# Optimization experiments

Hardware: AMD Instinct MI355X
Metric: run time of the kernel (lower is better)

## Reference

```python
import jax, jax.numpy as jnp
import numpy as np

T, B, S, K, C = 2, 64, 30, 12, 20
N_ITEMS, D_ITEM, D_RNN = 20000, 128, 256
D_IN = D_ITEM + D_RNN  # cross_mode concatenates h_meta to basket embedding


def gru_cell(x, h, Wih, Whh, bih, bhh):
    # PyTorch GRUCell gate order: r, z, n
    gi = x @ Wih.T + bih
    gh = h @ Whh.T + bhh
    ir, iz, in_ = jnp.split(gi, 3, -1)
    hr, hz, hn = jnp.split(gh, 3, -1)
    r = jax.nn.sigmoid(ir + hr)
    z = jax.nn.sigmoid(iz + hz)
    n = jnp.tanh(in_ + r * hn)
    return (1.0 - z) * n + z * h


def setup_inputs() -> dict:
    key = jax.random.key(0)
    ks = jax.random.split(key, 16)
    def u(k, sh, fan):
        b = 1.0 / np.sqrt(fan)
        return jax.random.uniform(k, sh, jnp.float32, -b, b)
    return {
        "user_vectors": jax.random.randint(ks[0], (B,), 0, 1000),
        "item_vectors": jax.random.randint(ks[1], (T, B, S, K), 0, N_ITEMS),
        "copy_vectors": jax.random.randint(ks[2], (T, B, S, C), 0, N_ITEMS),
        "emb": jax.random.normal(ks[3], (N_ITEMS, D_ITEM), jnp.float32) * 0.05,
        "Wih": u(ks[4], (T, 3 * D_RNN, D_IN), D_RNN),
        "Whh": u(ks[5], (T, 3 * D_RNN, D_RNN), D_RNN),
        "bih": u(ks[6], (T, 3 * D_RNN), D_RNN),
        "bhh": u(ks[7], (T, 3 * D_RNN), D_RNN),
        "mWih": u(ks[8], (3 * D_RNN, T * D_RNN), D_RNN),
        "mWhh": u(ks[9], (3 * D_RNN, D_RNN), D_RNN),
        "mbih": u(ks[10], (3 * D_RNN,), D_RNN),
        "mbhh": u(ks[11], (3 * D_RNN,), D_RNN),
        "Wnew": u(ks[12], (N_ITEMS, D_RNN), D_RNN),
        "bnew": u(ks[13], (N_ITEMS,), D_RNN),
        "Wcopy": u(ks[14], (T, N_ITEMS, D_RNN), D_RNN),
        "bcopy": u(ks[15], (T, N_ITEMS), D_RNN),
    }


def _forward(item_vectors, copy_vectors, emb, Wih, Whh, bih, bhh,
             mWih, mWhh, mbih, mbhh, Wnew, bnew, Wcopy, bcopy):
    emb = emb.at[0].set(0.0)  # padding_idx=0
    e_items = emb[item_vectors]                               # [T,B,S,K,Di]
    valid = (item_vectors > 0).astype(e_items.dtype)          # [T,B,S,K]
    n_basket = valid.sum(-1)                                  # [T,B,S]
    cell_mask = (n_basket > 0).astype(e_items.dtype)          # [T,B,S]
    den = n_basket + (n_basket == 0).astype(e_items.dtype)
    e_baskets = e_items.sum(-2) / den[..., None]              # ave pool [T,B,S,Di]

    xs = jnp.moveaxis(e_baskets, 2, 0)  # [S,T,B,Di]
    ms = jnp.moveaxis(cell_mask, 2, 0)  # [S,T,B]

    h0 = jnp.zeros((T, B, D_RNN), e_items.dtype)
    hm0 = jnp.zeros((B, D_RNN), e_items.dtype)
    task_gru = jax.vmap(gru_cell)  # vmap over the task axis (distinct weights)

    def step(carry, inp):
        h_tasks, h_meta = carry
        x_t, m_t = inp
        # cross_mode: concat current meta hidden onto each task's input
        cell_in = jnp.concatenate(
            [x_t, jnp.broadcast_to(h_meta, (T, B, D_RNN))], -1)  # [T,B,D_IN]
        nh = task_gru(cell_in, h_tasks, Wih, Whh, bih, bhh)
        m = m_t[..., None]
        h_tasks = nh * m + h_tasks * (1.0 - m)  # freeze hidden on empty baskets
        meta_in = jnp.transpose(h_tasks, (1, 0, 2)).reshape(B, T * D_RNN)
        h_meta = gru_cell(meta_in, h_meta, mWih, mWhh, mbih, mbhh)
        return (h_tasks, h_meta), (h_tasks, h_meta)

    _, (h_seq, hm_seq) = jax.lax.scan(step, (h0, hm0), (xs, ms))
    e_rnn_tasks = jnp.transpose(h_seq, (1, 2, 0, 3))  # [T,B,S,H]
    e_rnn_meta = jnp.transpose(hm_seq, (1, 0, 2))     # [B,S,H]

    score_new = jnp.einsum('bsh,nh->bsn', e_rnn_meta, Wnew) + bnew  # [B,S,N]
    ti = jnp.arange(T)[:, None, None, None]
    bi = jnp.arange(B)[None, :, None, None]
    si = jnp.arange(S)[None, None, :, None]
    copy_mask = jnp.zeros((T, B, S, N_ITEMS), score_new.dtype).at[
        ti, bi, si, copy_vectors].set(1.0)  # scatter_(-1, copy_vectors, 1)
    score_copy = (jnp.einsum('tbsh,tnh->tbsn', e_rnn_tasks, Wcopy)
                  + bcopy[:, None, None, :]) * copy_mask  # [T,B,S,N]
    # stack new-item scores with per-task masked copy scores
    return jnp.concatenate([score_new[None], score_copy], 0)  # [T+1,B,S,N]


def reference(user_vectors, item_vectors, copy_vectors, emb, Wih, Whh, bih, bhh,
              mWih, mWhh, mbih, mbhh, Wnew, bnew, Wcopy, bcopy):
    return _forward(item_vectors, copy_vectors, emb, Wih, Whh, bih, bhh,
                    mWih, mWhh, mbih, mbhh, Wnew, bnew, Wcopy, bcopy)
```

## Files before the change

### kernel.cpp

```cpp
#include <hip/hip_runtime.h>

typedef unsigned short u16;
typedef unsigned int u32;
typedef unsigned long long u64;
typedef __attribute__((ext_vector_type(8))) short short8;
typedef __attribute__((ext_vector_type(4))) float f32x4;

#define NB_ 64
#define NHELP_ 6195

static __device__ __forceinline__ f32x4 mfma16(short8 a, short8 b, f32x4 c) {
  return __builtin_amdgcn_mfma_f32_16x16x32_bf16(a, b, c, 0, 0, 0);
}

static __device__ __forceinline__ void split_bf16(float x, u16& hi, u16& lo) {
  unsigned u = __float_as_uint(x);
  unsigned r = (u + 0x7fffu + ((u >> 16) & 1u)) >> 16;
  hi = (u16)r;
  float fh = __uint_as_float(r << 16);
  float xl = x - fh;
  unsigned ul = __float_as_uint(xl);
  unsigned rl2 = (ul + 0x7fffu + ((ul >> 16) & 1u)) >> 16;
  lo = (u16)rl2;
}

static __device__ __forceinline__ void astore(u32* p, u32 v) {
  __hip_atomic_store(p, v, __ATOMIC_RELAXED, __HIP_MEMORY_SCOPE_AGENT);
}
static __device__ __forceinline__ void unpack8(const uint4& a, const uint4& b,
                                               short8& h, short8& l) {
  u32 wb[8] = {a.x, a.y, a.z, a.w, b.x, b.y, b.z, b.w};
  #pragma unroll
  for (int j = 0; j < 8; ++j) {
    h[j] = (short)(wb[j] & 0xffffu);
    l[j] = (short)(wb[j] >> 16);
  }
}
static __device__ __forceinline__ float unpack_hl(u32 pk) {
  return __uint_as_float((pk & 0xffffu) << 16) + __uint_as_float(pk & 0xffff0000u);
}
static __device__ __forceinline__ void vload8(const u32* p, short8& h, short8& l) {
  uint4 a = *(const uint4*)p;
  uint4 b = *(const uint4*)(p + 4);
  unpack8(a, b, h, l);
}

__global__ __launch_bounds__(256) void k_prep(const int* __restrict__ iv,
                                              const float* __restrict__ emb,
                                              u16* __restrict__ ebh, u16* __restrict__ ebl,
                                              float* __restrict__ cm,
                                              const float* __restrict__ Wih,
                                              const float* __restrict__ Whh,
                                              const float* __restrict__ mWih,
                                              const float* __restrict__ mWhh,
                                              const float* __restrict__ Wnew,
                                              u16* __restrict__ w1h, u16* __restrict__ w1l,
                                              u16* __restrict__ w2h, u16* __restrict__ w2l,
                                              u16* __restrict__ wnh, u16* __restrict__ wnl) {
  if (blockIdx.x < 1920) {
    int u = blockIdx.x * 2 + (threadIdx.x >> 7);
    int s = u >> 7;
    int t = (u >> 6) & 1;
    int b = u & 63;
    int d = threadIdx.x & 127;
    const int ibase = ((t * 64 + b) * 30 + s) * 12;
    float sum = 0.f;
    int cnt = 0;
    for (int k = 0; k < 12; ++k) {
      int idx = iv[ibase + k];
      if (idx > 0) { cnt++; sum += emb[(size_t)idx * 128 + d]; }
    }
    float den = (cnt > 0) ? (float)cnt : 1.f;
    float v = sum / den;
    u16 hi, lo; split_bf16(v, hi, lo);
    ebh[(size_t)u * 128 + d] = hi;
    ebl[(size_t)u * 128 + d] = lo;
    if (d == 0) cm[u] = (cnt > 0) ? 1.f : 0.f;
    return;
  }
  int gu = (blockIdx.x - 1920) * 4 + (threadIdx.x >> 6);
  int lane = threadIdx.x & 63;
  int ko = (lane >> 4) * 8;
  int cl = lane & 15;
  float src[8];
  if (gu < 2560) {
    int blk = gu / 40, r = gu % 40, ksIdx = r >> 1, nt = r & 1;
    int t = blk >> 5, hd0 = (blk & 31) * 8;
    int c = nt * 16 + cl;
    if (c < 24) {
      int gc = (c < 8) ? (hd0 + c) : (c < 16) ? (256 + hd0 + (c - 8)) : (512 + hd0 + (c - 16));
      const float* wrow; int kk;
      if (ksIdx < 8)       { wrow = Wih + (size_t)(t * 768 + gc) * 384 + 128; kk = ksIdx * 32 + ko; }
      else if (ksIdx < 16) { wrow = Whh + (size_t)(t * 768 + gc) * 256;       kk = (ksIdx - 8) * 32 + ko; }
      else                 { wrow = Wih + (size_t)(t * 768 + gc) * 384;       kk = (ksIdx - 16) * 32 + ko; }
      #pragma unroll
      for (int j = 0; j < 8; ++j) src[j] = wrow[kk + j];
    } else {
      #pragma unroll
      for (int j = 0; j < 8; ++j) src[j] = 0.f;
    }
    int off = gu * 512 + lane * 8;
    #pragma unroll
    for (int j = 0; j < 8; ++j) { u16 h, l; split_bf16(src[j], h, l); w1h[off + j] = h; w1l[off + j] = l; }
  } else if (gu < 4096) {
    int g2 = gu - 2560;
    int blk = g2 / 24, ksIdx = g2 % 24;
    int t1 = blk >> 5;
    int hd0 = blk * 4;
    int c = cl;
    if (c < 12) {
      int gc = (c < 4) ? (hd0 + c) : (c < 8) ? (256 + hd0 + (c - 4)) : (512 + hd0 + (c - 8));
      if (ksIdx < 16) {
        int chunk = (ksIdx < 8) ? (t1 * 8 + ksIdx) : ((1 - t1) * 8 + (ksIdx - 8));
        int kk = chunk * 32 + ko;
        #pragma unroll
        for (int j = 0; j < 8; ++j) src[j] = mWih[(size_t)gc * 512 + kk + j];
      } else {
        int kk = (ksIdx - 16) * 32 + ko;
        #pragma unroll
        for (int j = 0; j < 8; ++j) src[j] = mWhh[(size_t)gc * 256 + kk + j];
      }
    } else {
      #pragma unroll
      for (int j = 0; j < 8; ++j) src[j] = 0.f;
    }
    int off = g2 * 512 + lane * 8;
    #pragma unroll
    for (int j = 0; j < 8; ++j) { u16 h, l; split_bf16(src[j], h, l); w2h[off + j] = h; w2l[off + j] = l; }
  } else if (gu < 14144) {
    int g3 = gu - 4096;
    int gnt = g3 >> 3, ks = g3 & 7;
    int col = gnt * 16 + cl;
    if (col < 20000) {
      int kk = ks * 32 + ko;
      #pragma unroll
      for (int j = 0; j < 8; ++j) src[j] = Wnew[(size_t)col * 256 + kk + j];
    } else {
      #pragma unroll
      for (int j = 0; j < 8; ++j) src[j] = 0.f;
    }
    int off = g3 * 512 + lane * 8;
    #pragma unroll
    for (int j = 0; j < 8; ++j) { u16 h, l; split_bf16(src[j], h, l); wnh[off + j] = h; wnl[off + j] = l; }
  }
}

__global__ __launch_bounds__(256) void k_gix(const u16* __restrict__ ebh, const u16* __restrict__ ebl,
                                             const u16* __restrict__ w1h, const u16* __restrict__ w1l,
                                             const float* __restrict__ bih, const float* __restrict__ bhh,
                                             float* __restrict__ gix) {
  int blk = blockIdx.x;
  int t1 = blk >> 5, hd1 = (blk & 31) * 8;
  int tid = threadIdx.x, lane = tid & 63, w = tid >> 6;
  int arow = w * 16 + (lane & 15);
  int ko = (lane >> 4) * 8;
  __shared__ u16 lwh[4096], lwl[4096];
  {
    const uint4* sh = (const uint4*)(w1h + ((size_t)blk * 40 + 32) * 512);
    const uint4* sl = (const uint4*)(w1l + ((size_t)blk * 40 + 32) * 512);
    uint4* dh = (uint4*)lwh; uint4* dl = (uint4*)lwl;
    for (int i = tid; i < 512; i += 256) { dh[i] = sh[i]; dl[i] = sl[i]; }
  }
  int c = lane & 15;
  float brz, bn = 0.f;
  {
    int gc = (c < 8) ? (hd1 + c) : (256 + hd1 + (c - 8));
    brz = bih[t1 * 768 + gc] + bhh[t1 * 768 + gc];
    if (c < 8) bn = bih[t1 * 768 + 512 + hd1 + c];
  }
  __syncthreads();
  for (int s = 0; s < 30; ++s) {
    f32x4 a3[2];
    a3[0] = (f32x4){0.f, 0.f, 0.f, 0.f};
    a3[1] = (f32x4){0.f, 0.f, 0.f, 0.f};
    const u16* Xh = ebh + (size_t)((s * 2 + t1) * 64 + arow) * 128;
    const u16* Xl = ebl + (size_t)((s * 2 + t1) * 64 + arow) * 128;
    #pragma unroll
    for (int k = 0; k < 4; ++k) {
      short8 xh = *(const short8*)(Xh + k * 32 + ko);
      short8 xl = *(const short8*)(Xl + k * 32 + ko);
      #pragma unroll
      for (int nt = 0; nt < 2; ++nt) {
        short8 bh = *(const short8*)(lwh + (k * 2 + nt) * 512 + lane * 8);
        short8 bl = *(const short8*)(lwl + (k * 2 + nt) * 512 + lane * 8);
        a3[nt] = mfma16(xh, bh, a3[nt]);
        a3[nt] = mfma16(xl, bh, a3[nt]);
        a3[nt] = mfma16(xh, bl, a3[nt]);
      }
    }
    float* grow = gix + (size_t)(blk * 30 + s) * 64 * 32;
    #pragma unroll
    for (int i = 0; i < 4; ++i) {
      int r = w * 16 + (lane >> 4) * 4 + i;
      grow[r * 32 + c] = a3[0][i] + brz;
      if (c < 8) grow[r * 32 + 16 + c] = a3[1][i] + bn;
    }
  }
}

static __device__ __forceinline__ void bar_arrive(u32* slots, int blk, int epoch) {
  __syncthreads();
  if (threadIdx.x == 0) astore(slots + blk, (u32)epoch);
}
static __device__ __forceinline__ void bar_wait(u32* slots, int epoch) {
  int lane = threadIdx.x & 63;
  u32 v;
  for (;;) {
    asm volatile("global_load_dword %0, %1, off sc0 sc1\n\ts_waitcnt vmcnt(0)"
                 : "=v"(v) : "v"(slots + lane) : "memory");
    if ((int)v >= epoch) break;
  }
}
static __device__ __forceinline__ void helper_wait(const u32* hprog, int target) {
  if (threadIdx.x == 0) {
    u32 v;
    for (;;) {
      asm volatile("global_load_dword %0, %1, off sc0 sc1\n\ts_waitcnt vmcnt(0)"
                   : "=v"(v) : "v"(hprog) : "memory");
      if ((int)v >= target) break;
      __builtin_amdgcn_s_sleep(15);
      __builtin_amdgcn_s_sleep(15);
    }
  }
  __syncthreads();
}

#define RNN_LDS 130560

__global__ __launch_bounds__(256, 1) void k_mega(
    const u16* __restrict__ w1h, const u16* __restrict__ w1l,
    const u16* __restrict__ w2h, const u16* __restrict__ w2l,
    const float* __restrict__ gix,
    const float* __restrict__ bhh,
    const float* __restrict__ mbih, const float* __restrict__ mbhh,
    const float* __restrict__ cm,
    u32* __restrict__ hpk,
    u32* __restrict__ apk,
    u32* slots,
    const u16* __restrict__ wnh, const u16* __restrict__ wnl,
    const float* __restrict__ bnew,
    const int* __restrict__ cv,
    const float* __restrict__ wc,
    const float* __restrict__ bc,
    float* __restrict__ out) {
  u32* hprog = slots + 64;

  if (blockIdx.x >= NB_) {
    int h = blockIdx.x - NB_;
    int g = h / 413, r = h % 413;
    int tid = threadIdx.x, lane = tid & 63, w = tid >> 6;
    int ko = (lane >> 4) * 8;
    if (r < 256) {
      int s = 2 * g + (r >= 128);
      int rr = r & 127;
      int t = rr >> 6, b = rr & 63;
      float* orow = out + (size_t)(1 + t) * 38400000 + (size_t)(b * 30 + s) * 20000;
      f32x4 z4 = {0.f, 0.f, 0.f, 0.f};
      f32x4* zp = (f32x4*)orow;
      for (int i = tid; i < 5000; i += 256)
        __builtin_nontemporal_store(z4, zp + i);
      helper_wait(hprog, 2 * s + 1);
      const u32* hp = hpk + (size_t)(((s + 1) * 2 + t) * 64 + b) * 256;
      uint4 hq = *(const uint4*)(hp + lane * 4);
      float4 h4;
      h4.x = unpack_hl(hq.x); h4.y = unpack_hl(hq.y);
      h4.z = unpack_hl(hq.z); h4.w = unpack_hl(hq.w);
      int base = ((t * 64 + b) * 30 + s) * 20;
      for (int c = w; c < 20; c += 4) {
        int idx = cv[base + c];
        const float* wr = wc + ((size_t)t * 20000 + idx) * 256;
        float4 w4 = *(const float4*)(wr + lane * 4);
        float d = h4.x * w4.x + h4.y * w4.y + h4.z * w4.z + h4.w * w4.w;
        #pragma unroll
        for (int m = 32; m >= 1; m >>= 1) d += __shfl_xor(d, m, 64);
        if (lane == 0) orow[idx] = d + bc[t * 20000 + idx];
      }
    } else {
      int q = g, nb = r - 256;
      helper_wait(hprog, 4 * q + 4);
      f32x4 acc[2][8];
      #pragma unroll
      for (int mi = 0; mi < 2; ++mi)
        #pragma unroll
        for (int nt = 0; nt < 8; ++nt) acc[mi][nt] = (f32x4){0.f, 0.f, 0.f, 0.f};
      #pragma unroll
      for (int ks = 0; ks < 8; ++ks) {
        short8 ah[2], al[2];
        #pragma unroll
        for (int mi = 0; mi < 2; ++mi) {
          int rrow = q * 128 + (w * 2 + mi) * 16 + (lane & 15);
          vload8(apk + (size_t)rrow * 256 + ks * 32 + ko, ah[mi], al[mi]);
        }
        #pragma unroll
        for (int nt = 0; nt < 8; ++nt) {
          int un = (nb * 8 + nt) * 8 + ks;
          short8 bh = *(const short8*)(wnh + (size_t)un * 512 + lane * 8);
          short8 bl = *(const short8*)(wnl + (size_t)un * 512 + lane * 8);
          #pragma unroll
          for (int mi = 0; mi < 2; ++mi) {
            acc[mi][nt] = mfma16(ah[mi], bh, acc[mi][nt]);
            acc[mi][nt] = mfma16(al[mi], bh, acc[mi][nt]);
            acc[mi][nt] = mfma16(ah[mi], bl, acc[mi][nt]);
          }
        }
      }
      #pragma unroll
      for (int mi = 0; mi < 2; ++mi)
        #pragma unroll
        for (int nt = 0; nt < 8; ++nt) {
          int col = nb * 128 + nt * 16 + (lane & 15);
          if (col < 20000) {
            float bn = bnew[col];
            #pragma unroll
            for (int i = 0; i < 4; ++i) {
              int rrow = q * 128 + (w * 2 + mi) * 16 + (lane >> 4) * 4 + i;
              int sA = rrow >> 6, bA = rrow & 63;
              out[(size_t)(bA * 30 + sA) * 20000 + col] = acc[mi][nt][i] + bn;
            }
          }
        }
    }
    return;
  }

  extern __shared__ char smem[];
  u16* lw1h = (u16*)smem;
  u16* lw1l = (u16*)(smem + 32768);
  u16* lw2h = (u16*)(smem + 65536);
  u16* lw2l = (u16*)(smem + 90112);
  float* ls_rz = (float*)(smem + 114688);
  float* ls_gi = (float*)(smem + 118784);
  float* ls_gh = (float*)(smem + 120832);
  float* ls_cm = (float*)(smem + 122880);

  const int blk = blockIdx.x;
  const int tid = threadIdx.x;
  const int lane = tid & 63;
  const int w = tid >> 6;
  const int t1 = blk >> 5;
  const int hd1 = (blk & 31) * 8;
  const int hd2 = blk * 4;
  const int arow = w * 16 + (lane & 15);
  const int ko = (lane >> 4) * 8;
  int epoch = 0;

  {
    const uint4* s1h = (const uint4*)(w1h + (size_t)blk * 40 * 512);
    const uint4* s1l = (const uint4*)(w1l + (size_t)blk * 40 * 512);
    uint4* d1h = (uint4*)lw1h; uint4* d1l = (uint4*)lw1l;
    for (int i = tid; i < 2048; i += 256) { d1h[i] = s1h[i]; d1l[i] = s1l[i]; }
    const uint4* s2h = (const uint4*)(w2h + (size_t)blk * 24 * 512);
    const uint4* s2l = (const uint4*)(w2l + (size_t)blk * 24 * 512);
    uint4* d2h = (uint4*)lw2h; uint4* d2l = (uint4*)lw2l;
    for (int i = tid; i < 1536; i += 256) { d2h[i] = s2h[i]; d2l[i] = s2l[i]; }
    for (int i = tid; i < 1920; i += 256) ls_cm[i] = cm[((i >> 6) * 2 + t1) * 64 + (i & 63)];
  }
  const int cc = lane & 15;
  float bhhn = (cc < 8) ? bhh[t1 * 768 + 512 + hd1 + cc] : 0.f;
  float mrz_b = 0.f, mgi_b = 0.f, mgh_b = 0.f;
  if (cc < 8) {
    int gc = (cc < 4) ? (hd2 + cc) : (256 + hd2 + (cc - 4));
    mrz_b = mbih[gc] + mbhh[gc];
  } else if (cc < 12) {
    int gn = 512 + hd2 + (cc - 8);
    mgi_b = mbih[gn];
    mgh_b = mbhh[gn];
  }

  float gq[8];
  {
    const float* grow = gix + (size_t)(blk * 30 + 0) * 2048;
    #pragma unroll
    for (int i = 0; i < 4; ++i) {
      int r = w * 16 + (lane >> 4) * 4 + i;
      gq[i]     = grow[r * 32 + cc];
      gq[4 + i] = grow[r * 32 + 16 + (cc & 7)];
    }
  }
  __syncthreads();

  short8 ah1[8], al1[8];
  short8 xh2[8], xl2[8];
  f32x4 a2s[2];
  a2s[0] = (f32x4){0.f, 0.f, 0.f, 0.f};
  a2s[1] = (f32x4){0.f, 0.f, 0.f, 0.f};
  float hold0 = 0.f, hold1 = 0.f;
  float hm_reg = 0.f;

  for (int s = 0; s < 30; ++s) {
    f32x4 a1[2];
    a1[0] = (f32x4){0.f, 0.f, 0.f, 0.f};
    a1[1] = (f32x4){0.f, 0.f, 0.f, 0.f};
    if (s > 0) {
      bar_wait(slots, epoch);
      if (blk == 0 && tid == 0) astore(hprog, (u32)epoch);
      const u32* Ap = apk + (size_t)((s - 1) * 64 + arow) * 256 + ko;
      uint4 ra[16];
      #pragma unroll
      for (int k = 0; k < 8; ++k) {
        ra[2 * k]     = *(const uint4*)(Ap + k * 32);
        ra[2 * k + 1] = *(const uint4*)(Ap + k * 32 + 4);
      }
      #pragma unroll
      for (int k = 0; k < 8; ++k) {
        unpack8(ra[2 * k], ra[2 * k + 1], ah1[k], al1[k]);
        #pragma unroll
        for (int nt = 0; nt < 2; ++nt) {
          short8 bh = *(const short8*)(lw1h + (k * 2 + nt) * 512 + lane * 8);
          short8 bl = *(const short8*)(lw1l + (k * 2 + nt) * 512 + lane * 8);
          a1[nt] = mfma16(ah1[k], bh, a1[nt]);
          a1[nt] = mfma16(al1[k], bh, a1[nt]);
          a1[nt] = mfma16(ah1[k], bl, a1[nt]);
        }
      }
    }
    #pragma unroll
    for (int i = 0; i < 4; ++i) {
      int rl = (lane >> 4) * 4 + i;
      ls_rz[(w * 16 + rl) * 16 + cc] = a1[0][i] + a2s[0][i] + gq[i];
      if (cc < 8) {
        ls_gi[(w * 16 + rl) * 8 + cc] = a1[1][i] + gq[4 + i];
        ls_gh[(w * 16 + rl) * 8 + cc] = a2s[1][i] + bhhn;
      }
    }
    asm volatile("s_waitcnt lgkmcnt(0)" ::: "memory");
    {
      int item = lane;
      int rl = item >> 3, c = item & 7;
      float rv = ls_rz[(w * 16 + rl) * 16 + c], zv = ls_rz[(w * 16 + rl) * 16 + 8 + c];
      float gi = ls_gi[(w * 16 + rl) * 8 + c], gh = ls_gh[(w * 16 + rl) * 8 + c];
      float r = 1.f / (1.f + expf(-rv));
      float z = 1.f / (1.f + expf(-zv));
      float n = tanhf(gi + r * gh);
      int b = w * 16 + rl;
      float m = ls_cm[s * 64 + b];
      float hnew = (1.f - z) * n + z * hold0;
      float hout = (m > 0.5f) ? hnew : hold0;
      hold0 = hout;
      int oo = (((s + 1) * 2 + t1) * 64 + b) * 256 + hd1 + c;
      u16 xh, xl; split_bf16(hout, xh, xl);
      astore(hpk + oo, (u32)xh | ((u32)xl << 16));
    }
    {
      int item = 64 + lane;
      int rl = item >> 3, c = item & 7;
      float rv = ls_rz[(w * 16 + rl) * 16 + c], zv = ls_rz[(w * 16 + rl) * 16 + 8 + c];
      float gi = ls_gi[(w * 16 + rl) * 8 + c], gh = ls_gh[(w * 16 + rl) * 8 + c];
      float r = 1.f / (1.f + expf(-rv));
      float z = 1.f / (1.f + expf(-zv));
      float n = tanhf(gi + r * gh);
      int b = w * 16 + rl;
      float m = ls_cm[s * 64 + b];
      float hnew = (1.f - z) * n + z * hold1;
      float hout = (m > 0.5f) ? hnew : hold1;
      hold1 = hout;
      int oo = (((s + 1) * 2 + t1) * 64 + b) * 256 + hd1 + c;
      u16 xh, xl; split_bf16(hout, xh, xl);
      astore(hpk + oo, (u32)xh | ((u32)xl << 16));
    }
    ++epoch;
    bar_arrive(slots, blk, epoch);

    f32x4 m1 = (f32x4){0.f, 0.f, 0.f, 0.f};
    f32x4 m2 = (f32x4){0.f, 0.f, 0.f, 0.f};
    if (s > 0) {
      #pragma unroll
      for (int k = 0; k < 8; ++k) {
        short8 bh = *(const short8*)(lw2h + (16 + k) * 512 + lane * 8);
        short8 bl = *(const short8*)(lw2l + (16 + k) * 512 + lane * 8);
        m2 = mfma16(ah1[k], bh, m2);
        m2 = mfma16(al1[k], bh, m2);
        m2 = mfma16(ah1[k], bl, m2);
      }
    }
    if (s < 29) {
      const float* grow = gix + (size_t)(blk * 30 + s + 1) * 2048;
      #pragma unroll
      for (int i = 0; i < 4; ++i) {
        int r = w * 16 + (lane >> 4) * 4 + i;
        gq[i]     = grow[r * 32 + cc];
        gq[4 + i] = grow[r * 32 + 16 + (cc & 7)];
      }
    }
    bar_wait(slots, epoch);
    if (blk == 0 && tid == 0) astore(hprog, (u32)epoch);

    {
      const u32* Hp = hpk + (size_t)(((s + 1) * 2 + t1) * 64 + arow) * 256 + ko;
      const u32* Hq = hpk + (size_t)(((s + 1) * 2 + (1 - t1)) * 64 + arow) * 256 + ko;
      uint4 rx[16], ry[16];
      #pragma unroll
      for (int k = 0; k < 8; ++k) {
        rx[2 * k]     = *(const uint4*)(Hp + k * 32);
        rx[2 * k + 1] = *(const uint4*)(Hp + k * 32 + 4);
        ry[2 * k]     = *(const uint4*)(Hq + k * 32);
        ry[2 * k + 1] = *(const uint4*)(Hq + k * 32 + 4);
      }
      #pragma unroll
      for (int k = 0; k < 8; ++k) {
        unpack8(rx[2 * k], rx[2 * k + 1], xh2[k], xl2[k]);
        short8 bh = *(const short8*)(lw2h + k * 512 + lane * 8);
        short8 bl = *(const short8*)(lw2l + k * 512 + lane * 8);
        m1 = mfma16(xh2[k], bh, m1);
        m1 = mfma16(xl2[k], bh, m1);
        m1 = mfma16(xh2[k], bl, m1);
      }
      #pragma unroll
      for (int k = 0; k < 8; ++k) {
        short8 yh, yl;
        unpack8(ry[2 * k], ry[2 * k + 1], yh, yl);
        short8 bh = *(const short8*)(lw2h + (8 + k) * 512 + lane * 8);
        short8 bl = *(const short8*)(lw2l + (8 + k) * 512 + lane * 8);
        m1 = mfma16(yh, bh, m1);
        m1 = mfma16(yl, bh, m1);
        m1 = mfma16(yh, bl, m1);
      }
    }
    #pragma unroll
    for (int i = 0; i < 4; ++i) {
      int rl = (lane >> 4) * 4 + i;
      if (cc < 8) {
        ls_rz[(w * 16 + rl) * 16 + cc] = m1[i] + m2[i] + mrz_b;
      } else if (cc < 12) {
        ls_gi[(w * 16 + rl) * 8 + (cc - 8)] = m1[i] + mgi_b;
        ls_gh[(w * 16 + rl) * 8 + (cc - 8)] = m2[i] + mgh_b;
      }
    }
    asm volatile("s_waitcnt lgkmcnt(0)" ::: "memory");
    {
      int rl = lane >> 2, c = lane & 3;
      float rv = ls_rz[(w * 16 + rl) * 16 + c], zv = ls_rz[(w * 16 + rl) * 16 + 4 + c];
      float gi = ls_gi[(w * 16 + rl) * 8 + c], gh = ls_gh[(w * 16 + rl) * 8 + c];
      float r = 1.f / (1.f + expf(-rv));
      float z = 1.f / (1.f + expf(-zv));
      float n = tanhf(gi + r * gh);
      int b = w * 16 + rl;
      int g2 = hd2 + c;
      float hmnew = (1.f - z) * n + z * hm_reg;
      hm_reg = hmnew;
      int ar = s * 64 + b;
      u16 xh, xl; split_bf16(hmnew, xh, xl);
      astore(apk + ar * 256 + g2, (u32)xh | ((u32)xl << 16));
    }
    ++epoch;
    bar_arrive(slots, blk, epoch);

    a2s[0] = (f32x4){0.f, 0.f, 0.f, 0.f};
    a2s[1] = (f32x4){0.f, 0.f, 0.f, 0.f};
    if (s < 29) {
      #pragma unroll
      for (int k = 0; k < 8; ++k) {
        #pragma unroll
        for (int nt = 0; nt < 2; ++nt) {
          short8 bh = *(const short8*)(lw1h + ((8 + k) * 2 + nt) * 512 + lane * 8);
          short8 bl = *(const short8*)(lw1l + ((8 + k) * 2 + nt) * 512 + lane * 8);
          a2s[nt] = mfma16(xh2[k], bh, a2s[nt]);
          a2s[nt] = mfma16(xl2[k], bh, a2s[nt]);
          a2s[nt] = mfma16(xh2[k], bl, a2s[nt]);
        }
      }
    }
  }
  if (blk == 0) {
    bar_wait(slots, epoch);
    if (tid == 0) astore(hprog, (u32)epoch);
  }
}

extern "C" void kernel_launch(void* const* d_in, const int* in_sizes, int n_in,
                              void* d_out, int out_size, void* d_ws, size_t ws_size,
                              hipStream_t stream) {
  const int* iv = (const int*)d_in[1];
  const int* cv = (const int*)d_in[2];
  const float* emb = (const float*)d_in[3];
  const float* Wih = (const float*)d_in[4];
  const float* Whh = (const float*)d_in[5];
  const float* bih = (const float*)d_in[6];
  const float* bhh = (const float*)d_in[7];
  const float* mWih = (const float*)d_in[8];
  const float* mWhh = (const float*)d_in[9];
  const float* mbih = (const float*)d_in[10];
  const float* mbhh = (const float*)d_in[11];
  const float* Wnew = (const float*)d_in[12];
  const float* bnew = (const float*)d_in[13];
  const float* Wcopy = (const float*)d_in[14];
  const float* bcopy = (const float*)d_in[15];
  float* out = (float*)d_out;
  char* ws = (char*)d_ws;

  size_t o = 0;
  auto take = [&](size_t sz) { size_t r = o; o += sz; return r; };
  size_t BAR = take(512);
  size_t CM  = take(15360);
  size_t EBH = take(983040);
  size_t EBL = take(983040);
  size_t HPK = take(4063232);
  size_t APK = take(1966080);
  size_t GIX = take(15728640);
  size_t W1H = take(2621440);
  size_t W1L = take(2621440);
  size_t W2H = take(1572864);
  size_t W2L = take(1572864);
  size_t WNH = take(10289152);
  size_t WNL = take(10289152);
  if (ws_size < o) return;

  hipFuncSetAttribute(reinterpret_cast<const void*>(k_mega),
                      hipFuncAttributeMaxDynamicSharedMemorySize, RNN_LDS);

  hipMemsetAsync(ws + BAR, 0, 512, stream);

  k_prep<<<5456, 256, 0, stream>>>(iv, emb, (u16*)(ws + EBH), (u16*)(ws + EBL), (float*)(ws + CM),
                                   Wih, Whh, mWih, mWhh, Wnew,
                                   (u16*)(ws + W1H), (u16*)(ws + W1L),
                                   (u16*)(ws + W2H), (u16*)(ws + W2L),
                                   (u16*)(ws + WNH), (u16*)(ws + WNL));
  k_gix<<<64, 256, 0, stream>>>((const u16*)(ws + EBH), (const u16*)(ws + EBL),
                                (const u16*)(ws + W1H), (const u16*)(ws + W1L),
                                bih, bhh, (float*)(ws + GIX));
  k_mega<<<NB_ + NHELP_, 256, RNN_LDS, stream>>>(
      (const u16*)(ws + W1H), (const u16*)(ws + W1L),
      (const u16*)(ws + W2H), (const u16*)(ws + W2L),
      (const float*)(ws + GIX), bhh, mbih, mbhh,
      (const float*)(ws + CM),
      (u32*)(ws + HPK), (u32*)(ws + APK),
      (u32*)(ws + BAR),
      (const u16*)(ws + WNH), (const u16*)(ws + WNL),
      bnew, cv, Wcopy, bcopy, out);
}
```

Baseline: 473.1 us.

## Fuse input-gate precompute kernel into persistent RNN megakernel

Removes the separate k_gix launch and computes the input-side gate projections inside each RNN block of k_mega, reusing W1 slices now kept in a larger LDS region. Each block writes and then reads back its own gix rows, which saves a kernel launch and the reload of W1 from global memory. Helper blocks that zero the copy-score rows now wait for RNN progress before zeroing, which shifts when that bandwidth is used. The cost is more LDS per RNN block and a longer serial prologue before the recurrence starts.

```diff
diff --git a/kernel.cpp b/kernel.cpp
--- a/kernel.cpp
+++ b/kernel.cpp
@@ -145,59 +145,6 @@
   }
 }
 
-__global__ __launch_bounds__(256) void k_gix(const u16* __restrict__ ebh, const u16* __restrict__ ebl,
-                                             const u16* __restrict__ w1h, const u16* __restrict__ w1l,
-                                             const float* __restrict__ bih, const float* __restrict__ bhh,
-                                             float* __restrict__ gix) {
-  int blk = blockIdx.x;
-  int t1 = blk >> 5, hd1 = (blk & 31) * 8;
-  int tid = threadIdx.x, lane = tid & 63, w = tid >> 6;
-  int arow = w * 16 + (lane & 15);
-  int ko = (lane >> 4) * 8;
-  __shared__ u16 lwh[4096], lwl[4096];
-  {
-    const uint4* sh = (const uint4*)(w1h + ((size_t)blk * 40 + 32) * 512);
-    const uint4* sl = (const uint4*)(w1l + ((size_t)blk * 40 + 32) * 512);
-    uint4* dh = (uint4*)lwh; uint4* dl = (uint4*)lwl;
-    for (int i = tid; i < 512; i += 256) { dh[i] = sh[i]; dl[i] = sl[i]; }
-  }
-  int c = lane & 15;
-  float brz, bn = 0.f;
-  {
-    int gc = (c < 8) ? (hd1 + c) : (256 + hd1 + (c - 8));
-    brz = bih[t1 * 768 + gc] + bhh[t1 * 768 + gc];
-    if (c < 8) bn = bih[t1 * 768 + 512 + hd1 + c];
-  }
-  __syncthreads();
-  for (int s = 0; s < 30; ++s) {
-    f32x4 a3[2];
-    a3[0] = (f32x4){0.f, 0.f, 0.f, 0.f};
-    a3[1] = (f32x4){0.f, 0.f, 0.f, 0.f};
-    const u16* Xh = ebh + (size_t)((s * 2 + t1) * 64 + arow) * 128;
-    const u16* Xl = ebl + (size_t)((s * 2 + t1) * 64 + arow) * 128;
-    #pragma unroll
-    for (int k = 0; k < 4; ++k) {
-      short8 xh = *(const short8*)(Xh + k * 32 + ko);
-      short8 xl = *(const short8*)(Xl + k * 32 + ko);
-      #pragma unroll
-      for (int nt = 0; nt < 2; ++nt) {
-        short8 bh = *(const short8*)(lwh + (k * 2 + nt) * 512 + lane * 8);
-        short8 bl = *(const short8*)(lwl + (k * 2 + nt) * 512 + lane * 8);
-        a3[nt] = mfma16(xh, bh, a3[nt]);
-        a3[nt] = mfma16(xl, bh, a3[nt]);
-        a3[nt] = mfma16(xh, bl, a3[nt]);
-      }
-    }
-    float* grow = gix + (size_t)(blk * 30 + s) * 64 * 32;
-    #pragma unroll
-    for (int i = 0; i < 4; ++i) {
-      int r = w * 16 + (lane >> 4) * 4 + i;
-      grow[r * 32 + c] = a3[0][i] + brz;
-      if (c < 8) grow[r * 32 + 16 + c] = a3[1][i] + bn;
-    }
-  }
-}
-
 static __device__ __forceinline__ void bar_arrive(u32* slots, int blk, int epoch) {
   __syncthreads();
   if (threadIdx.x == 0) astore(slots + blk, (u32)epoch);
@@ -225,13 +172,14 @@
   __syncthreads();
 }
 
-#define RNN_LDS 130560
+#define RNN_LDS 146944
 
 __global__ __launch_bounds__(256, 1) void k_mega(
     const u16* __restrict__ w1h, const u16* __restrict__ w1l,
     const u16* __restrict__ w2h, const u16* __restrict__ w2l,
-    const float* __restrict__ gix,
-    const float* __restrict__ bhh,
+    const u16* __restrict__ ebh, const u16* __restrict__ ebl,
+    float* __restrict__ gix,
+    const float* __restrict__ bih, const float* __restrict__ bhh,
     const float* __restrict__ mbih, const float* __restrict__ mbhh,
     const float* __restrict__ cm,
     u32* __restrict__ hpk,
@@ -255,16 +203,17 @@
       int rr = r & 127;
       int t = rr >> 6, b = rr & 63;
       float* orow = out + (size_t)(1 + t) * 38400000 + (size_t)(b * 30 + s) * 20000;
+      helper_wait(hprog, 2 * s + 1);
       f32x4 z4 = {0.f, 0.f, 0.f, 0.f};
       f32x4* zp = (f32x4*)orow;
       for (int i = tid; i < 5000; i += 256)
         __builtin_nontemporal_store(z4, zp + i);
-      helper_wait(hprog, 2 * s + 1);
       const u32* hp = hpk + (size_t)(((s + 1) * 2 + t) * 64 + b) * 256;
       uint4 hq = *(const uint4*)(hp + lane * 4);
       float4 h4;
       h4.x = unpack_hl(hq.x); h4.y = unpack_hl(hq.y);
       h4.z = unpack_hl(hq.z); h4.w = unpack_hl(hq.w);
+      __syncthreads();
       int base = ((t * 64 + b) * 30 + s) * 20;
       for (int c = w; c < 20; c += 4) {
         int idx = cv[base + c];
@@ -325,13 +274,13 @@
 
   extern __shared__ char smem[];
   u16* lw1h = (u16*)smem;
-  u16* lw1l = (u16*)(smem + 32768);
-  u16* lw2h = (u16*)(smem + 65536);
-  u16* lw2l = (u16*)(smem + 90112);
-  float* ls_rz = (float*)(smem + 114688);
-  float* ls_gi = (float*)(smem + 118784);
-  float* ls_gh = (float*)(smem + 120832);
-  float* ls_cm = (float*)(smem + 122880);
+  u16* lw1l = (u16*)(smem + 40960);
+  u16* lw2h = (u16*)(smem + 81920);
+  u16* lw2l = (u16*)(smem + 106496);
+  float* ls_rz = (float*)(smem + 131072);
+  float* ls_gi = (float*)(smem + 135168);
+  float* ls_gh = (float*)(smem + 137216);
+  float* ls_cm = (float*)(smem + 139264);
 
   const int blk = blockIdx.x;
   const int tid = threadIdx.x;
@@ -348,7 +297,7 @@
     const uint4* s1h = (const uint4*)(w1h + (size_t)blk * 40 * 512);
     const uint4* s1l = (const uint4*)(w1l + (size_t)blk * 40 * 512);
     uint4* d1h = (uint4*)lw1h; uint4* d1l = (uint4*)lw1l;
-    for (int i = tid; i < 2048; i += 256) { d1h[i] = s1h[i]; d1l[i] = s1l[i]; }
+    for (int i = tid; i < 2560; i += 256) { d1h[i] = s1h[i]; d1l[i] = s1l[i]; }
     const uint4* s2h = (const uint4*)(w2h + (size_t)blk * 24 * 512);
     const uint4* s2l = (const uint4*)(w2l + (size_t)blk * 24 * 512);
     uint4* d2h = (uint4*)lw2h; uint4* d2l = (uint4*)lw2l;
@@ -366,6 +315,43 @@
     mgi_b = mbih[gn];
     mgh_b = mbhh[gn];
   }
+  float brz_g, bn_g = 0.f;
+  {
+    int gc = (cc < 8) ? (hd1 + cc) : (256 + hd1 + (cc - 8));
+    brz_g = bih[t1 * 768 + gc] + bhh[t1 * 768 + gc];
+    if (cc < 8) bn_g = bih[t1 * 768 + 512 + hd1 + cc];
+  }
+  __syncthreads();
+
+  for (int s = 0; s < 30; ++s) {
+    f32x4 a3[2];
+    a3[0] = (f32x4){0.f, 0.f, 0.f, 0.f};
+    a3[1] = (f32x4){0.f, 0.f, 0.f, 0.f};
+    const u16* Xh = ebh + (size_t)((s * 2 + t1) * 64 + arow) * 128;
+    const u16* Xl = ebl + (size_t)((s * 2 + t1) * 64 + arow) * 128;
+    #pragma unroll
+    for (int k = 0; k < 4; ++k) {
+      short8 xh = *(const short8*)(Xh + k * 32 + ko);
+      short8 xl = *(const short8*)(Xl + k * 32 + ko);
+      #pragma unroll
+      for (int nt = 0; nt < 2; ++nt) {
+        int un = (16 + k) * 2 + nt;
+        short8 bh = *(const short8*)(lw1h + un * 512 + lane * 8);
+        short8 bl = *(const short8*)(lw1l + un * 512 + lane * 8);
+        a3[nt] = mfma16(xh, bh, a3[nt]);
+        a3[nt] = mfma16(xl, bh, a3[nt]);
+        a3[nt] = mfma16(xh, bl, a3[nt]);
+      }
+    }
+    float* grow = gix + (size_t)(blk * 30 + s) * 2048;
+    #pragma unroll
+    for (int i = 0; i < 4; ++i) {
+      int r = w * 16 + (lane >> 4) * 4 + i;
+      grow[r * 32 + cc] = a3[0][i] + brz_g;
+      if (cc < 8) grow[r * 32 + 16 + cc] = a3[1][i] + bn_g;
+    }
+  }
+  __syncthreads();
 
   float gq[8];
   {
@@ -377,7 +363,6 @@
       gq[4 + i] = grow[r * 32 + 16 + (cc & 7)];
     }
   }
-  __syncthreads();
 
   short8 ah1[8], al1[8];
   short8 xh2[8], xl2[8];
@@ -615,13 +600,12 @@
                                    (u16*)(ws + W1H), (u16*)(ws + W1L),
                                    (u16*)(ws + W2H), (u16*)(ws + W2L),
                                    (u16*)(ws + WNH), (u16*)(ws + WNL));
-  k_gix<<<64, 256, 0, stream>>>((const u16*)(ws + EBH), (const u16*)(ws + EBL),
-                                (const u16*)(ws + W1H), (const u16*)(ws + W1L),
-                                bih, bhh, (float*)(ws + GIX));
   k_mega<<<NB_ + NHELP_, 256, RNN_LDS, stream>>>(
       (const u16*)(ws + W1H), (const u16*)(ws + W1L),
       (const u16*)(ws + W2H), (const u16*)(ws + W2L),
-      (const float*)(ws + GIX), bhh, mbih, mbhh,
+      (const u16*)(ws + EBH), (const u16*)(ws + EBL),
+      (float*)(ws + GIX),
+      bih, bhh, mbih, mbhh,
       (const float*)(ws + CM),
       (u32*)(ws + HPK), (u32*)(ws + APK),
       (u32*)(ws + BAR),
```

New measurement: 474.6 us. No clear change (+0.3%).

## Enlarge new-score GEMM tiles to 256 rows and regroup helper blocks

Applied to the files above, without the earlier changes.

Helper blocks computing score_new now process 256 rows (4 M-subtiles per wave) per 128-column tile instead of 128 rows, halving the number of GEMM helper blocks and reusing each loaded Wnew fragment across twice as many rows. The copy-score zeroing blocks are regrouped in sets of four timesteps, with a tail group for the last two steps and a final 2-subtile GEMM. This cuts redundant weight loads and block count, but each GEMM block waits for more RNN steps before it can start, which reduces overlap with the recurrence and raises register pressure.

```diff
diff --git a/kernel.cpp b/kernel.cpp
--- a/kernel.cpp
+++ b/kernel.cpp
@@ -7,7 +7,7 @@
 typedef __attribute__((ext_vector_type(4))) float f32x4;
 
 #define NB_ 64
-#define NHELP_ 6195
+#define NHELP_ 5096
 
 static __device__ __forceinline__ f32x4 mfma16(short8 a, short8 b, f32x4 c) {
   return __builtin_amdgcn_mfma_f32_16x16x32_bf16(a, b, c, 0, 0, 0);
@@ -225,6 +225,58 @@
   __syncthreads();
 }
 
+template<int MI>
+static __device__ __forceinline__ void gnew_tile(int rowbase, int nb, int tid,
+                                                 const u32* __restrict__ apk,
+                                                 const u16* __restrict__ wnh,
+                                                 const u16* __restrict__ wnl,
+                                                 const float* __restrict__ bnew,
+                                                 float* __restrict__ out) {
+  int lane = tid & 63, w = tid >> 6;
+  int ko = (lane >> 4) * 8;
+  f32x4 acc[MI][8];
+  #pragma unroll
+  for (int mi = 0; mi < MI; ++mi)
+    #pragma unroll
+    for (int nt = 0; nt < 8; ++nt) acc[mi][nt] = (f32x4){0.f, 0.f, 0.f, 0.f};
+  #pragma unroll
+  for (int ks = 0; ks < 8; ++ks) {
+    short8 ah[MI], al[MI];
+    #pragma unroll
+    for (int mi = 0; mi < MI; ++mi) {
+      int rrow = rowbase + (w * MI + mi) * 16 + (lane & 15);
+      vload8(apk + (size_t)rrow * 256 + ks * 32 + ko, ah[mi], al[mi]);
+    }
+    #pragma unroll
+    for (int nt = 0; nt < 8; ++nt) {
+      int un = (nb * 8 + nt) * 8 + ks;
+      short8 bh = *(const short8*)(wnh + (size_t)un * 512 + lane * 8);
+      short8 bl = *(const short8*)(wnl + (size_t)un * 512 + lane * 8);
+      #pragma unroll
+      for (int mi = 0; mi < MI; ++mi) {
+        acc[mi][nt] = mfma16(ah[mi], bh, acc[mi][nt]);
+        acc[mi][nt] = mfma16(al[mi], bh, acc[mi][nt]);
+        acc[mi][nt] = mfma16(ah[mi], bl, acc[mi][nt]);
+      }
+    }
+  }
+  #pragma unroll
+  for (int mi = 0; mi < MI; ++mi)
+    #pragma unroll
+    for (int nt = 0; nt < 8; ++nt) {
+      int col = nb * 128 + nt * 16 + (lane & 15);
+      if (col < 20000) {
+        float bn = bnew[col];
+        #pragma unroll
+        for (int i = 0; i < 4; ++i) {
+          int rrow = rowbase + (w * MI + mi) * 16 + (lane >> 4) * 4 + i;
+          int sA = rrow >> 6, bA = rrow & 63;
+          out[(size_t)(bA * 30 + sA) * 20000 + col] = acc[mi][nt][i] + bn;
+        }
+      }
+    }
+}
+
 #define RNN_LDS 130560
 
 __global__ __launch_bounds__(256, 1) void k_mega(
@@ -247,12 +299,18 @@
 
   if (blockIdx.x >= NB_) {
     int h = blockIdx.x - NB_;
-    int g = h / 413, r = h % 413;
     int tid = threadIdx.x, lane = tid & 63, w = tid >> 6;
-    int ko = (lane >> 4) * 8;
-    if (r < 256) {
-      int s = 2 * g + (r >= 128);
-      int rr = r & 127;
+    int s = -1, rr = 0, q = -1, nb = 0;
+    if (h < 4683) {
+      int g = h / 669, r = h % 669;
+      if (r < 512) { s = 4 * g + (r >> 7); rr = r & 127; }
+      else         { q = g; nb = r - 512; }
+    } else {
+      int h2 = h - 4683;
+      if (h2 < 256) { s = 28 + (h2 >> 7); rr = h2 & 127; }
+      else          { q = 7; nb = h2 - 256; }
+    }
+    if (s >= 0) {
       int t = rr >> 6, b = rr & 63;
       float* orow = out + (size_t)(1 + t) * 38400000 + (size_t)(b * 30 + s) * 20000;
       f32x4 z4 = {0.f, 0.f, 0.f, 0.f};
@@ -275,50 +333,12 @@
         for (int m = 32; m >= 1; m >>= 1) d += __shfl_xor(d, m, 64);
         if (lane == 0) orow[idx] = d + bc[t * 20000 + idx];
       }
+    } else if (q < 7) {
+      helper_wait(hprog, 8 * q + 8);
+      gnew_tile<4>(q * 256, nb, tid, apk, wnh, wnl, bnew, out);
     } else {
-      int q = g, nb = r - 256;
-      helper_wait(hprog, 4 * q + 4);
-      f32x4 acc[2][8];
-      #pragma unroll
-      for (int mi = 0; mi < 2; ++mi)
-        #pragma unroll
-        for (int nt = 0; nt < 8; ++nt) acc[mi][nt] = (f32x4){0.f, 0.f, 0.f, 0.f};
-      #pragma unroll
-      for (int ks = 0; ks < 8; ++ks) {
-        short8 ah[2], al[2];
-        #pragma unroll
-        for (int mi = 0; mi < 2; ++mi) {
-          int rrow = q * 128 + (w * 2 + mi) * 16 + (lane & 15);
-          vload8(apk + (size_t)rrow * 256 + ks * 32 + ko, ah[mi], al[mi]);
-        }
-        #pragma unroll
-        for (int nt = 0; nt < 8; ++nt) {
-          int un = (nb * 8 + nt) * 8 + ks;
-          short8 bh = *(const short8*)(wnh + (size_t)un * 512 + lane * 8);
-          short8 bl = *(const short8*)(wnl + (size_t)un * 512 + lane * 8);
-          #pragma unroll
-          for (int mi = 0; mi < 2; ++mi) {
-            acc[mi][nt] = mfma16(ah[mi], bh, acc[mi][nt]);
-            acc[mi][nt] = mfma16(al[mi], bh, acc[mi][nt]);
-            acc[mi][nt] = mfma16(ah[mi], bl, acc[mi][nt]);
-          }
-        }
-      }
-      #pragma unroll
-      for (int mi = 0; mi < 2; ++mi)
-        #pragma unroll
-        for (int nt = 0; nt < 8; ++nt) {
-          int col = nb * 128 + nt * 16 + (lane & 15);
-          if (col < 20000) {
-            float bn = bnew[col];
-            #pragma unroll
-            for (int i = 0; i < 4; ++i) {
-              int rrow = q * 128 + (w * 2 + mi) * 16 + (lane >> 4) * 4 + i;
-              int sA = rrow >> 6, bA = rrow & 63;
-              out[(size_t)(bA * 30 + sA) * 20000 + col] = acc[mi][nt][i] + bn;
-            }
-          }
-        }
+      helper_wait(hprog, 60);
+      gnew_tile<2>(1792, nb, tid, apk, wnh, wnl, bnew, out);
     }
     return;
   }
```

Result: no change. 465.1 us, median of 2 (-1.7%).
